# Kernel tuning notes

Measured on AMD Instinct MI355X. Metric: run time of the kernel, lower is better.

The kernel has to match this reference:

```python
import jax, jax.numpy as jnp
import numpy as np

DIM = 1024
HIDDEN = 4096
N_EXPERTS = 8
K = 2
TEMP = 1.0


def setup_inputs() -> dict:
    key = jax.random.key(0)
    ks = jax.random.split(key, 7)
    s = 0.02
    x = jax.random.normal(ks[0], (4, 2048, DIM), dtype=jnp.float32)
    router_w = jax.random.normal(ks[1], (N_EXPERTS, DIM), dtype=jnp.float32) * s
    router_b = jnp.zeros((N_EXPERTS,), dtype=jnp.float32)
    # Expert(dim, hidden, 'swiglu'): fc1: dim -> 2*hidden, fc2: hidden -> dim
    w1 = jax.random.normal(ks[2], (N_EXPERTS, 2 * HIDDEN, DIM), dtype=jnp.float32) * s
    b1 = jnp.zeros((N_EXPERTS, 2 * HIDDEN), dtype=jnp.float32)
    w2 = jax.random.normal(ks[3], (N_EXPERTS, DIM, HIDDEN), dtype=jnp.float32) * s
    b2 = jnp.zeros((N_EXPERTS, DIM), dtype=jnp.float32)
    return {"x": x, "router_w": router_w, "router_b": router_b,
            "w1": w1, "b1": b1, "w2": w2, "b2": b2}


def _expert_ffn(xf, wa, ba, wb, bb):
    # xf: [T, dim]; swiglu FFN
    h = xf @ wa.T + ba                       # [T, 2*hidden]
    h1, h2 = jnp.split(h, 2, axis=-1)
    h = jax.nn.silu(h1) * h2                 # [T, hidden]
    return h @ wb.T + bb                     # [T, dim]


def reference(x, router_w, router_b, w1, b1, w2, b2):
    b, t, d = x.shape
    logits = (x @ router_w.T + router_b) / TEMP          # [b, t, E]
    topk_val, topk_idx = jax.lax.top_k(logits, K)        # [b, t, K]
    weights = jax.nn.softmax(topk_val, axis=-1)          # [b, t, K]

    xf = x.reshape(-1, d)                                # [T, dim]
    # Compute every expert on all tokens (dense reference for irregular dispatch)
    outs = jax.vmap(_expert_ffn, in_axes=(None, 0, 0, 0, 0))(xf, w1, b1, w2, b2)  # [E, T, dim]
    outs = jnp.transpose(outs, (1, 0, 2))                # [T, E, dim]

    idx = topk_idx.reshape(-1, K)                        # [T, K]
    gathered = jnp.take_along_axis(outs, idx[:, :, None], axis=1)  # [T, K, dim]
    combined = (gathered * weights.reshape(-1, K, 1)).sum(axis=1)  # [T, dim]
    return combined.reshape(b, t, d)
```

## Files before the change

### kernel.cpp

```cpp
#include <hip/hip_runtime.h>

#define T_TOK 8192
#define DIMX 1024
#define HID 4096
#define NE 8
#define TP (T_TOK * 2)
#define PADR 128
#define BK 64

typedef unsigned short ushort_t;
typedef __attribute__((ext_vector_type(4))) float f32x4;
typedef __attribute__((ext_vector_type(8))) short bf16x8;
typedef __attribute__((ext_vector_type(8))) unsigned short u16x8;

__device__ __forceinline__ ushort_t f2bf(float f) {
    unsigned u = __float_as_uint(f);
    u += 0x7FFFu + ((u >> 16) & 1u);
    return (ushort_t)(u >> 16);
}
__device__ __forceinline__ float b2f(ushort_t h) {
    return __uint_as_float(((unsigned)h) << 16);
}

__device__ __forceinline__ void gload_lds16(const void* g, void* l) {
    __builtin_amdgcn_global_load_lds((const __attribute__((address_space(1))) void*)g,
                                     (__attribute__((address_space(3))) void*)l, 16, 0, 0);
}

__device__ __forceinline__ f32x4 mfma16(bf16x8 a, bf16x8 b, f32x4 c) {
    return __builtin_amdgcn_mfma_f32_16x16x32_bf16(a, b, c, 0, 0, 0);
}


__global__ __launch_bounds__(256) void router_kernel(
    const float* __restrict__ x, const float* __restrict__ rw, const float* __restrict__ rb,
    int* __restrict__ topk_idx, float* __restrict__ topk_w)
{
    __shared__ float s_rw[NE * DIMX];
    int tid = threadIdx.x;
    for (int i = tid * 4; i < NE * DIMX; i += 1024) {
        float4 v = *(const float4*)(rw + i);
        *(float4*)(s_rw + i) = v;
    }
    __syncthreads();
    int lane = tid & 63, wid = tid >> 6;
    int t = blockIdx.x * 4 + wid;
    const float* xr = x + (size_t)t * DIMX;
    float acc[NE];
#pragma unroll
    for (int e = 0; e < NE; e++) acc[e] = 0.f;
    for (int j = 0; j < DIMX; j += 64) {
        float xv = xr[j + lane];
#pragma unroll
        for (int e = 0; e < NE; e++) acc[e] += xv * s_rw[e * DIMX + j + lane];
    }
#pragma unroll
    for (int e = 0; e < NE; e++) {
#pragma unroll
        for (int off = 32; off > 0; off >>= 1) acc[e] += __shfl_xor(acc[e], off, 64);
    }
    if (lane == 0) {
        float v[NE];
#pragma unroll
        for (int e = 0; e < NE; e++) v[e] = acc[e] + rb[e];
        int i0 = 0; float b0 = v[0];
#pragma unroll
        for (int e = 1; e < NE; e++) if (v[e] > b0) { b0 = v[e]; i0 = e; }
        int i1 = -1; float b1v = -1e30f;
#pragma unroll
        for (int e = 0; e < NE; e++) if (e != i0 && v[e] > b1v) { b1v = v[e]; i1 = e; }
        float ex = __expf(b1v - b0);
        float inv = 1.f / (1.f + ex);
        topk_idx[t * 2]     = i0;  topk_idx[t * 2 + 1] = i1;
        topk_w[t * 2]       = inv; topk_w[t * 2 + 1]   = ex * inv;
    }
}

__global__ __launch_bounds__(256) void prefix_kernel(
    const int* __restrict__ topk_idx, int* __restrict__ counts,
    int* __restrict__ offsets, int* __restrict__ cursor)
{
    __shared__ int hist[NE * 256];
    int tid = threadIdx.x;
    int loc[NE];
#pragma unroll
    for (int e = 0; e < NE; e++) loc[e] = 0;
    for (int i = tid; i < TP; i += 256) loc[topk_idx[i]]++;
#pragma unroll
    for (int e = 0; e < NE; e++) hist[e * 256 + tid] = loc[e];
    __syncthreads();
    if (tid < NE) {
        int s = 0;
        for (int j = 0; j < 256; j++) s += hist[tid * 256 + j];
        counts[tid] = s;
        cursor[tid] = 0;
    }
    __syncthreads();
    if (tid == 0) {
        int s = 0;
        for (int e = 0; e < NE; e++) { offsets[e] = s; s += counts[e]; }
    }
}

__global__ __launch_bounds__(256) void sg_kernel(
    const float* __restrict__ x, const int* __restrict__ topk_idx,
    const float* __restrict__ topk_w, const int* __restrict__ offsets,
    int* __restrict__ cursor, ushort_t* __restrict__ Xp,
    float* __restrict__ w_of, int* __restrict__ slot_of)
{
    __shared__ int s_pos[2];
    int t = blockIdx.x;
    if (threadIdx.x == 0) {
        int e0 = topk_idx[2 * t], e1 = topk_idx[2 * t + 1];
        int p0 = offsets[e0] + atomicAdd(&cursor[e0], 1);
        int p1 = offsets[e1] + atomicAdd(&cursor[e1], 1);
        s_pos[0] = p0; s_pos[1] = p1;
        w_of[p0] = topk_w[2 * t]; w_of[p1] = topk_w[2 * t + 1];
        slot_of[2 * t] = p0; slot_of[2 * t + 1] = p1;
    }
    __syncthreads();
    int p0 = s_pos[0], p1 = s_pos[1];
    int i = threadIdx.x;
    float4 v = ((const float4*)(x + (size_t)t * DIMX))[i];
    ushort4 o = make_ushort4(f2bf(v.x), f2bf(v.y), f2bf(v.z), f2bf(v.w));
    ((ushort4*)(Xp + (size_t)p0 * DIMX))[i] = o;
    ((ushort4*)(Xp + (size_t)p1 * DIMX))[i] = o;
}


__global__ __launch_bounds__(256) void cvt_kernel(
    const float* __restrict__ w1, ushort_t* __restrict__ w1d,
    const float* __restrict__ w2, ushort_t* __restrict__ w2d)
{
    const int n8_w1 = NE * 2 * HID * DIMX / 8;
    const int n8_tot = n8_w1 + NE * DIMX * HID / 8;
    int stride = gridDim.x * 256;
    for (int i = blockIdx.x * 256 + threadIdx.x; i < n8_tot; i += stride) {
        const float* src; ushort_t* dst; int j;
        if (i < n8_w1) { src = w1; dst = w1d; j = i; }
        else           { src = w2; dst = w2d; j = i - n8_w1; }
        float4 a = ((const float4*)src)[j * 2];
        float4 b = ((const float4*)src)[j * 2 + 1];
        u16x8 o = { f2bf(a.x), f2bf(a.y), f2bf(a.z), f2bf(a.w),
                    f2bf(b.x), f2bf(b.y), f2bf(b.z), f2bf(b.w) };
        ((u16x8*)dst)[j] = o;
    }
}

__global__ __launch_bounds__(256, 2) void fc1_kernel(
    const ushort_t* __restrict__ Xp, const ushort_t* __restrict__ w1b,
    const float* __restrict__ b1,
    const int* __restrict__ counts, const int* __restrict__ offsets,
    ushort_t* __restrict__ H)
{
    const int wg = blockIdx.x;
    const int e  = wg & 7;
    const int r  = wg >> 3;
    const int band = r >> 9;
    const int rem  = r & 511;
    const int nt   = rem >> 3;
    const int mt   = band * 8 + (rem & 7);

    const int cnt = counts[e];
    if (mt * 128 >= cnt) return;
    const int base = offsets[e] + mt * 128;
    int rows_valid = cnt - mt * 128; if (rows_valid > 128) rows_valid = 128;

    __shared__ ushort_t As[128 * BK];
    __shared__ ushort_t Bs1[64 * BK];
    __shared__ ushort_t Bs2[64 * BK];

    const int tid = threadIdx.x, lane = tid & 63, wid = tid >> 6;
    const int wave_m = wid >> 1, wave_n = wid & 1;

    const ushort_t* Ag  = Xp + (size_t)base * DIMX;
    const ushort_t* B1g = w1b + ((size_t)e * 2 * HID + (size_t)nt * 64) * DIMX;
    const ushort_t* B2g = B1g + (size_t)HID * DIMX;

    const ushort_t* agp[4]; ushort_t* alp[4];
#pragma unroll
    for (int i = 0; i < 4; i++) {
        int s = wid * 4 + i;
        int r2 = s * 8 + (lane >> 3);
        int c = (lane & 7) ^ (r2 & 7);
        agp[i] = Ag + (size_t)r2 * DIMX + c * 8;
        alp[i] = As + s * 512 + lane * 8;
    }
    const ushort_t* bgp[4]; ushort_t* blp[4];
#pragma unroll
    for (int i = 0; i < 2; i++) {
        int s = wid * 2 + i;
        int r2 = s * 8 + (lane >> 3);
        int c = (lane & 7) ^ (r2 & 7);
        bgp[i]     = B1g + (size_t)r2 * DIMX + c * 8;
        blp[i]     = Bs1 + s * 512 + lane * 8;
        bgp[2 + i] = B2g + (size_t)r2 * DIMX + c * 8;
        blp[2 + i] = Bs2 + s * 512 + lane * 8;
    }

    f32x4 acc1[4][2], acc2[4][2];
#pragma unroll
    for (int mf = 0; mf < 4; mf++)
#pragma unroll
        for (int nf = 0; nf < 2; nf++) {
            acc1[mf][nf] = (f32x4){0.f, 0.f, 0.f, 0.f};
            acc2[mf][nf] = (f32x4){0.f, 0.f, 0.f, 0.f};
        }

    const int q = lane >> 4, rA = lane & 15;
    for (int ko = 0; ko < DIMX / BK; ko++) {
#pragma unroll
        for (int i = 0; i < 4; i++) gload_lds16(agp[i], alp[i]);
#pragma unroll
        for (int i = 0; i < 4; i++) gload_lds16(bgp[i], blp[i]);
#pragma unroll
        for (int i = 0; i < 4; i++) { agp[i] += BK; bgp[i] += BK; }
        __syncthreads();

        bf16x8 af[4][2], bf1[2][2], bf2[2][2];
#pragma unroll
        for (int mf = 0; mf < 4; mf++) {
            int r2 = wave_m * 64 + mf * 16 + rA;
            const ushort_t* rp = As + r2 * BK;
            af[mf][0] = *(const bf16x8*)(rp + ((q    ) ^ (r2 & 7)) * 8);
            af[mf][1] = *(const bf16x8*)(rp + ((q + 4) ^ (r2 & 7)) * 8);
        }
#pragma unroll
        for (int nf = 0; nf < 2; nf++) {
            int r2 = wave_n * 32 + nf * 16 + rA;
            const ushort_t* rp1 = Bs1 + r2 * BK;
            const ushort_t* rp2 = Bs2 + r2 * BK;
            bf1[nf][0] = *(const bf16x8*)(rp1 + ((q    ) ^ (r2 & 7)) * 8);
            bf1[nf][1] = *(const bf16x8*)(rp1 + ((q + 4) ^ (r2 & 7)) * 8);
            bf2[nf][0] = *(const bf16x8*)(rp2 + ((q    ) ^ (r2 & 7)) * 8);
            bf2[nf][1] = *(const bf16x8*)(rp2 + ((q + 4) ^ (r2 & 7)) * 8);
        }
#pragma unroll
        for (int mf = 0; mf < 4; mf++)
#pragma unroll
            for (int nf = 0; nf < 2; nf++) {
                acc1[mf][nf] = mfma16(af[mf][0], bf1[nf][0], acc1[mf][nf]);
                acc1[mf][nf] = mfma16(af[mf][1], bf1[nf][1], acc1[mf][nf]);
                acc2[mf][nf] = mfma16(af[mf][0], bf2[nf][0], acc2[mf][nf]);
                acc2[mf][nf] = mfma16(af[mf][1], bf2[nf][1], acc2[mf][nf]);
            }
        __syncthreads();
    }

    const float* b1p = b1 + (size_t)e * 2 * HID + (size_t)nt * 64;
    const bool full = (rows_valid == 128);
#pragma unroll
    for (int mf = 0; mf < 4; mf++) {
#pragma unroll
        for (int nf = 0; nf < 2; nf++) {
            int col = wave_n * 32 + nf * 16 + rA;
            float bb1 = b1p[col];
            float bb2 = b1p[HID + col];
#pragma unroll
            for (int rr = 0; rr < 4; rr++) {
                int row = wave_m * 64 + mf * 16 + q * 4 + rr;
                if (full || row < rows_valid) {
                    float v1 = acc1[mf][nf][rr] + bb1;
                    float v2 = acc2[mf][nf][rr] + bb2;
                    float hv = v1 * v2 / (1.f + __expf(-v1));
                    H[(size_t)(base + row) * HID + (size_t)nt * 64 + col] = f2bf(hv);
                }
            }
        }
    }
}

__global__ __launch_bounds__(256, 2) void fc2_kernel(
    const ushort_t* __restrict__ H, const ushort_t* __restrict__ w2b,
    const float* __restrict__ b2,
    const int* __restrict__ counts, const int* __restrict__ offsets,
    const float* __restrict__ w_of, ushort_t* __restrict__ Os)
{
    const int wg = blockIdx.x;
    const int e  = wg & 7;
    const int r  = wg >> 3;
    const int nt = r >> 5;
    const int mt = r & 31;

    const int cnt = counts[e];
    if (mt * 128 >= cnt) return;
    const int base = offsets[e] + mt * 128;
    int rows_valid = cnt - mt * 128; if (rows_valid > 128) rows_valid = 128;

    __shared__ ushort_t As[128 * BK];
    __shared__ ushort_t Bs[128 * BK];

    const int tid = threadIdx.x, lane = tid & 63, wid = tid >> 6;
    const int wave_m = wid >> 1, wave_n = wid & 1;

    const ushort_t* Ag = H + (size_t)base * HID;
    const ushort_t* Bg = w2b + ((size_t)e * DIMX + (size_t)nt * 128) * HID;

    const ushort_t* agp[4]; ushort_t* alp[4];
    const ushort_t* bgp[4]; ushort_t* blp[4];
#pragma unroll
    for (int i = 0; i < 4; i++) {
        int s = wid * 4 + i;
        int r2 = s * 8 + (lane >> 3);
        int c = (lane & 7) ^ (r2 & 7);
        agp[i] = Ag + (size_t)r2 * HID + c * 8;
        alp[i] = As + s * 512 + lane * 8;
        bgp[i] = Bg + (size_t)r2 * HID + c * 8;
        blp[i] = Bs + s * 512 + lane * 8;
    }

    f32x4 acc[4][4];
#pragma unroll
    for (int mf = 0; mf < 4; mf++)
#pragma unroll
        for (int nf = 0; nf < 4; nf++) acc[mf][nf] = (f32x4){0.f, 0.f, 0.f, 0.f};

    const int q = lane >> 4, rA = lane & 15;
    for (int ko = 0; ko < HID / BK; ko++) {
#pragma unroll
        for (int i = 0; i < 4; i++) gload_lds16(agp[i], alp[i]);
#pragma unroll
        for (int i = 0; i < 4; i++) gload_lds16(bgp[i], blp[i]);
#pragma unroll
        for (int i = 0; i < 4; i++) { agp[i] += BK; bgp[i] += BK; }
        __syncthreads();

        bf16x8 af[4][2], bfr[4][2];
#pragma unroll
        for (int mf = 0; mf < 4; mf++) {
            int r2 = wave_m * 64 + mf * 16 + rA;
            const ushort_t* rp = As + r2 * BK;
            af[mf][0] = *(const bf16x8*)(rp + ((q    ) ^ (r2 & 7)) * 8);
            af[mf][1] = *(const bf16x8*)(rp + ((q + 4) ^ (r2 & 7)) * 8);
        }
#pragma unroll
        for (int nf = 0; nf < 4; nf++) {
            int r2 = wave_n * 64 + nf * 16 + rA;
            const ushort_t* rp = Bs + r2 * BK;
            bfr[nf][0] = *(const bf16x8*)(rp + ((q    ) ^ (r2 & 7)) * 8);
            bfr[nf][1] = *(const bf16x8*)(rp + ((q + 4) ^ (r2 & 7)) * 8);
        }
#pragma unroll
        for (int mf = 0; mf < 4; mf++)
#pragma unroll
            for (int nf = 0; nf < 4; nf++) {
                acc[mf][nf] = mfma16(af[mf][0], bfr[nf][0], acc[mf][nf]);
                acc[mf][nf] = mfma16(af[mf][1], bfr[nf][1], acc[mf][nf]);
            }
        __syncthreads();
    }

    const float* b2p = b2 + (size_t)e * DIMX + (size_t)nt * 128;
    const bool full = (rows_valid == 128);
#pragma unroll
    for (int mf = 0; mf < 4; mf++) {
#pragma unroll
        for (int rr = 0; rr < 4; rr++) {
            int row = wave_m * 64 + mf * 16 + q * 4 + rr;
            if (full || row < rows_valid) {
                float wv = w_of[base + row];
#pragma unroll
                for (int nf = 0; nf < 4; nf++) {
                    int col = wave_n * 64 + nf * 16 + rA;
                    float val = (acc[mf][nf][rr] + b2p[col]) * wv;
                    Os[(size_t)(base + row) * DIMX + (size_t)nt * 128 + col] = f2bf(val);
                }
            }
        }
    }
}

__global__ __launch_bounds__(256) void combine_kernel(
    const ushort_t* __restrict__ Os, const int* __restrict__ slot_of, float* __restrict__ out)
{
    int t = blockIdx.x;
    int p0 = slot_of[t * 2], p1 = slot_of[t * 2 + 1];
    int i = threadIdx.x;
    ushort4 a = ((const ushort4*)(Os + (size_t)p0 * DIMX))[i];
    ushort4 b = ((const ushort4*)(Os + (size_t)p1 * DIMX))[i];
    float4 o;
    o.x = b2f(a.x) + b2f(b.x);
    o.y = b2f(a.y) + b2f(b.y);
    o.z = b2f(a.z) + b2f(b.z);
    o.w = b2f(a.w) + b2f(b.w);
    ((float4*)(out + (size_t)t * DIMX))[i] = o;
}


extern "C" void kernel_launch(void* const* d_in, const int* in_sizes, int n_in,
                              void* d_out, int out_size, void* d_ws, size_t ws_size,
                              hipStream_t stream) {
    (void)in_sizes; (void)n_in; (void)out_size; (void)ws_size;
    const float* x  = (const float*)d_in[0];
    const float* rw = (const float*)d_in[1];
    const float* rb = (const float*)d_in[2];
    const float* w1 = (const float*)d_in[3];
    const float* b1 = (const float*)d_in[4];
    const float* w2 = (const float*)d_in[5];
    const float* b2 = (const float*)d_in[6];
    float* out = (float*)d_out;

    char* p = (char*)d_ws;
    ushort_t* w1b = (ushort_t*)p; p += (size_t)NE * 2 * HID * DIMX * 2;
    ushort_t* w2b = (ushort_t*)p; p += (size_t)NE * DIMX * HID * 2;
    ushort_t* Xp  = (ushort_t*)p; p += (size_t)(TP + PADR) * DIMX * 2;
    ushort_t* Hb  = (ushort_t*)p; p += (size_t)(TP + PADR) * HID * 2;
    int* ints     = (int*)p;      p += 24 * sizeof(int);
    int*   counts  = ints;
    int*   cursor  = ints + 8;
    int*   offsets = ints + 16;
    int*   topk_idx = (int*)p;   p += (size_t)TP * 4;
    float* topk_w   = (float*)p; p += (size_t)TP * 4;
    float* w_of     = (float*)p; p += (size_t)TP * 4;
    int*   slot_of  = (int*)p;   p += (size_t)TP * 4;
    ushort_t* Os = Xp;

    router_kernel<<<T_TOK / 4, 256, 0, stream>>>(x, rw, rb, topk_idx, topk_w);
    prefix_kernel<<<1, 256, 0, stream>>>(topk_idx, counts, offsets, cursor);
    sg_kernel<<<T_TOK, 256, 0, stream>>>(x, topk_idx, topk_w, offsets, cursor,
                                         Xp, w_of, slot_of);
    cvt_kernel<<<2048, 256, 0, stream>>>(w1, w1b, w2, w2b);

    fc1_kernel<<<NE * 32 * 64, 256, 0, stream>>>(Xp, w1b, b1, counts, offsets, Hb);
    fc2_kernel<<<NE * 8 * 32, 256, 0, stream>>>(Hb, w2b, b2, counts, offsets, w_of, Os);
    combine_kernel<<<T_TOK, 256, 0, stream>>>(Os, slot_of, out);
}
```

Before: 1.283 ms.

## Double-buffer LDS tiles in fc1 and fc2 GEMM loops to overlap loads

Measured after the change: 1.580 ms. 23.2% more time.

```diff
diff --git a/kernel.cpp b/kernel.cpp
--- a/kernel.cpp
+++ b/kernel.cpp
@@ -166,9 +166,9 @@
     const int base = offsets[e] + mt * 128;
     int rows_valid = cnt - mt * 128; if (rows_valid > 128) rows_valid = 128;
 
-    __shared__ ushort_t As[128 * BK];
-    __shared__ ushort_t Bs1[64 * BK];
-    __shared__ ushort_t Bs2[64 * BK];
+    __shared__ ushort_t As[2 * 128 * BK];
+    __shared__ ushort_t Bs1[2 * 64 * BK];
+    __shared__ ushort_t Bs2[2 * 64 * BK];
 
     const int tid = threadIdx.x, lane = tid & 63, wid = tid >> 6;
     const int wave_m = wid >> 1, wave_n = wid & 1;
@@ -177,26 +177,37 @@
     const ushort_t* B1g = w1b + ((size_t)e * 2 * HID + (size_t)nt * 64) * DIMX;
     const ushort_t* B2g = B1g + (size_t)HID * DIMX;
 
-    const ushort_t* agp[4]; ushort_t* alp[4];
+    const ushort_t* agp[4]; int aoff[4];
 #pragma unroll
     for (int i = 0; i < 4; i++) {
         int s = wid * 4 + i;
         int r2 = s * 8 + (lane >> 3);
         int c = (lane & 7) ^ (r2 & 7);
         agp[i] = Ag + (size_t)r2 * DIMX + c * 8;
-        alp[i] = As + s * 512 + lane * 8;
-    }
-    const ushort_t* bgp[4]; ushort_t* blp[4];
+        aoff[i] = s * 512 + lane * 8;
+    }
+    const ushort_t* bgp[4]; int boff[4];
 #pragma unroll
     for (int i = 0; i < 2; i++) {
         int s = wid * 2 + i;
         int r2 = s * 8 + (lane >> 3);
         int c = (lane & 7) ^ (r2 & 7);
         bgp[i]     = B1g + (size_t)r2 * DIMX + c * 8;
-        blp[i]     = Bs1 + s * 512 + lane * 8;
+        boff[i]     = s * 512 + lane * 8;
         bgp[2 + i] = B2g + (size_t)r2 * DIMX + c * 8;
-        blp[2 + i] = Bs2 + s * 512 + lane * 8;
-    }
+        boff[2 + i] = s * 512 + lane * 8;
+    }
+
+#define FC1_STAGE(SEL) do {                                                   \
+        _Pragma("unroll")                                                     \
+        for (int i = 0; i < 4; i++) gload_lds16(agp[i], As + (SEL) * 8192 + aoff[i]); \
+        gload_lds16(bgp[0], Bs1 + (SEL) * 4096 + boff[0]);                    \
+        gload_lds16(bgp[1], Bs1 + (SEL) * 4096 + boff[1]);                    \
+        gload_lds16(bgp[2], Bs2 + (SEL) * 4096 + boff[2]);                    \
+        gload_lds16(bgp[3], Bs2 + (SEL) * 4096 + boff[3]);                    \
+        _Pragma("unroll")                                                     \
+        for (int i = 0; i < 4; i++) { agp[i] += BK; bgp[i] += BK; }           \
+    } while (0)
 
     f32x4 acc1[4][2], acc2[4][2];
 #pragma unroll
@@ -208,28 +219,30 @@
         }
 
     const int q = lane >> 4, rA = lane & 15;
+    FC1_STAGE(0);
+    __syncthreads();
+
     for (int ko = 0; ko < DIMX / BK; ko++) {
-#pragma unroll
-        for (int i = 0; i < 4; i++) gload_lds16(agp[i], alp[i]);
-#pragma unroll
-        for (int i = 0; i < 4; i++) gload_lds16(bgp[i], blp[i]);
-#pragma unroll
-        for (int i = 0; i < 4; i++) { agp[i] += BK; bgp[i] += BK; }
-        __syncthreads();
+        const int cur = ko & 1;
+        if (ko + 1 < DIMX / BK) FC1_STAGE(cur ^ 1);
+
+        const ushort_t* Ac  = As  + cur * 8192;
+        const ushort_t* B1c = Bs1 + cur * 4096;
+        const ushort_t* B2c = Bs2 + cur * 4096;
 
         bf16x8 af[4][2], bf1[2][2], bf2[2][2];
 #pragma unroll
         for (int mf = 0; mf < 4; mf++) {
             int r2 = wave_m * 64 + mf * 16 + rA;
-            const ushort_t* rp = As + r2 * BK;
+            const ushort_t* rp = Ac + r2 * BK;
             af[mf][0] = *(const bf16x8*)(rp + ((q    ) ^ (r2 & 7)) * 8);
             af[mf][1] = *(const bf16x8*)(rp + ((q + 4) ^ (r2 & 7)) * 8);
         }
 #pragma unroll
         for (int nf = 0; nf < 2; nf++) {
             int r2 = wave_n * 32 + nf * 16 + rA;
-            const ushort_t* rp1 = Bs1 + r2 * BK;
-            const ushort_t* rp2 = Bs2 + r2 * BK;
+            const ushort_t* rp1 = B1c + r2 * BK;
+            const ushort_t* rp2 = B2c + r2 * BK;
             bf1[nf][0] = *(const bf16x8*)(rp1 + ((q    ) ^ (r2 & 7)) * 8);
             bf1[nf][1] = *(const bf16x8*)(rp1 + ((q + 4) ^ (r2 & 7)) * 8);
             bf2[nf][0] = *(const bf16x8*)(rp2 + ((q    ) ^ (r2 & 7)) * 8);
@@ -287,8 +300,8 @@
     const int base = offsets[e] + mt * 128;
     int rows_valid = cnt - mt * 128; if (rows_valid > 128) rows_valid = 128;
 
-    __shared__ ushort_t As[128 * BK];
-    __shared__ ushort_t Bs[128 * BK];
+    __shared__ ushort_t As[2 * 128 * BK];
+    __shared__ ushort_t Bs[2 * 128 * BK];
 
     const int tid = threadIdx.x, lane = tid & 63, wid = tid >> 6;
     const int wave_m = wid >> 1, wave_n = wid & 1;
@@ -296,18 +309,26 @@
     const ushort_t* Ag = H + (size_t)base * HID;
     const ushort_t* Bg = w2b + ((size_t)e * DIMX + (size_t)nt * 128) * HID;
 
-    const ushort_t* agp[4]; ushort_t* alp[4];
-    const ushort_t* bgp[4]; ushort_t* blp[4];
+    const ushort_t* agp[4]; int aoff[4];
+    const ushort_t* bgp[4];
 #pragma unroll
     for (int i = 0; i < 4; i++) {
         int s = wid * 4 + i;
         int r2 = s * 8 + (lane >> 3);
         int c = (lane & 7) ^ (r2 & 7);
         agp[i] = Ag + (size_t)r2 * HID + c * 8;
-        alp[i] = As + s * 512 + lane * 8;
+        aoff[i] = s * 512 + lane * 8;
         bgp[i] = Bg + (size_t)r2 * HID + c * 8;
-        blp[i] = Bs + s * 512 + lane * 8;
-    }
+    }
+
+#define FC2_STAGE(SEL) do {                                                   \
+        _Pragma("unroll")                                                     \
+        for (int i = 0; i < 4; i++) gload_lds16(agp[i], As + (SEL) * 8192 + aoff[i]); \
+        _Pragma("unroll")                                                     \
+        for (int i = 0; i < 4; i++) gload_lds16(bgp[i], Bs + (SEL) * 8192 + aoff[i]); \
+        _Pragma("unroll")                                                     \
+        for (int i = 0; i < 4; i++) { agp[i] += BK; bgp[i] += BK; }           \
+    } while (0)
 
     f32x4 acc[4][4];
 #pragma unroll
@@ -316,27 +337,28 @@
         for (int nf = 0; nf < 4; nf++) acc[mf][nf] = (f32x4){0.f, 0.f, 0.f, 0.f};
 
     const int q = lane >> 4, rA = lane & 15;
+    FC2_STAGE(0);
+    __syncthreads();
+
     for (int ko = 0; ko < HID / BK; ko++) {
-#pragma unroll
-        for (int i = 0; i < 4; i++) gload_lds16(agp[i], alp[i]);
-#pragma unroll
-        for (int i = 0; i < 4; i++) gload_lds16(bgp[i], blp[i]);
-#pragma unroll
-        for (int i = 0; i < 4; i++) { agp[i] += BK; bgp[i] += BK; }
-        __syncthreads();
+        const int cur = ko & 1;
+        if (ko + 1 < HID / BK) FC2_STAGE(cur ^ 1);
+
+        const ushort_t* Ac = As + cur * 8192;
+        const ushort_t* Bc = Bs + cur * 8192;
 
         bf16x8 af[4][2], bfr[4][2];
 #pragma unroll
         for (int mf = 0; mf < 4; mf++) {
             int r2 = wave_m * 64 + mf * 16 + rA;
-            const ushort_t* rp = As + r2 * BK;
+            const ushort_t* rp = Ac + r2 * BK;
             af[mf][0] = *(const bf16x8*)(rp + ((q    ) ^ (r2 & 7)) * 8);
             af[mf][1] = *(const bf16x8*)(rp + ((q + 4) ^ (r2 & 7)) * 8);
         }
 #pragma unroll
         for (int nf = 0; nf < 4; nf++) {
             int r2 = wave_n * 64 + nf * 16 + rA;
-            const ushort_t* rp = Bs + r2 * BK;
+            const ushort_t* rp = Bc + r2 * BK;
             bfr[nf][0] = *(const bf16x8*)(rp + ((q    ) ^ (r2 & 7)) * 8);
             bfr[nf][1] = *(const bf16x8*)(rp + ((q + 4) ^ (r2 & 7)) * 8);
         }
```
